# Kernel optimization log

Measured on AMD Instinct MI355X. Metric: run time of the kernel, lower is better.

Reference implementation:

```python
import jax, jax.numpy as jnp
import numpy as np

KERNEL_SIZE = 5
KERNEL_NUM = 64
STRIDE = 1
PRIOR_VAR = 1.0


def setup_inputs() -> dict:
    key = jax.random.key(0)
    k1, k2 = jax.random.split(key)
    mu_in = jax.random.normal(k1, (128, 128, 128, 3), dtype=jnp.float32)
    # init: normal stddev 0.05 for w_mu, constant -4.6 for w_sigma
    w_mu = 0.05 * jax.random.normal(k2, (KERNEL_SIZE, KERNEL_SIZE, 3, KERNEL_NUM), dtype=jnp.float32)
    w_sigma = jnp.full((KERNEL_NUM,), -4.6, dtype=jnp.float32)
    return {"mu_in": mu_in, "w_mu": w_mu, "w_sigma": w_sigma}


def kl_regularizer_conv(mu, logvar):
    k = mu.shape[-1]
    mu2 = mu.reshape(-1, k)              # [k*k*C, kernel_num]
    n = mu2.shape[0]
    kl = -jnp.mean(1.0 + logvar
                   - jnp.log1p(jnp.exp(logvar)) / PRIOR_VAR
                   - jnp.sum(jnp.square(mu2), axis=0) / (n * PRIOR_VAR))
    kl = jnp.where(jnp.isnan(kl), jnp.float32(1e-05), kl)
    kl = jnp.where(jnp.isinf(kl), jnp.float32(1e-05), kl)
    return kl


def reference(mu_in, w_mu, w_sigma):
    B, H, W, C = mu_in.shape
    ks = KERNEL_SIZE
    kl_conv = kl_regularizer_conv(w_mu, w_sigma)
    w_sigma_2 = jnp.log1p(jnp.exp(w_sigma))  # softplus

    dn = ('NHWC', 'HWIO', 'NHWC')
    mu_out = jax.lax.conv_general_dilated(
        mu_in, w_mu, window_strides=(STRIDE, STRIDE), padding='VALID',
        dimension_numbers=dn)  # [B, Ho, Wo, kernel_num]

    # Per-patch sum of squares == sum-pool conv over squared input summed over C
    # (mathematically identical to extract_patches -> square -> sum, no im2col blowup)
    sq = jnp.sum(jnp.square(mu_in), axis=-1, keepdims=True)  # [B,H,W,1]
    ones_k = jnp.ones((ks, ks, 1, 1), dtype=mu_in.dtype)
    patch_ss = jax.lax.conv_general_dilated(
        sq, ones_k, window_strides=(STRIDE, STRIDE), padding='VALID',
        dimension_numbers=dn)  # [B, Ho, Wo, 1]
    x_dim = jnp.float32(ks * ks * C)
    # broadcast: softplus(w_sigma)[kn] * (sum_sq / x_dim)[B,Ho,Wo,1]
    Sigma_out = w_sigma_2 * (patch_ss / x_dim)  # [B, Ho, Wo, kernel_num]

    Ho = mu_out.shape[1]
    Sigma_out = Sigma_out.reshape(B, Ho, Ho, KERNEL_NUM)
    return (mu_out, Sigma_out, kl_conv)
```

## Files before the change

kernel.cpp:

```cpp
#include <hip/hip_runtime.h>
#include <hip/hip_bf16.h>
#include <math.h>

#define KS 5
#define CIN 3
#define KN 64
#define HIN 128
#define HO 124
#define ROWF (HIN * CIN)
#define NOUT (128LL * 124 * 124 * 64)
#define KP 104

typedef short bfrag8 __attribute__((ext_vector_type(8)));
typedef float ffrag4 __attribute__((ext_vector_type(4)));

__device__ __forceinline__ unsigned short f2bf(float f) {
    union { float f; unsigned u; } x;
    x.f = f;
    unsigned r = x.u + 0x7fffu + ((x.u >> 16) & 1u);
    return (unsigned short)(r >> 16);
}

__global__ void prep_kernel(const float* __restrict__ w_mu,
                            const float* __restrict__ w_sigma,
                            unsigned short* __restrict__ w_bf,
                            float* __restrict__ sp_out) {
    const int tid = threadIdx.x;
    const int n = tid >> 2;
    const int kbase = (tid & 3) * 26;
#pragma unroll
    for (int kk = 0; kk < 26; ++kk) {
        const int k = kbase + kk;
        float v = 0.f;
        if (k < 80) {
            const int r = k >> 4, t = k & 15;
            if (t < 15) v = w_mu[(r * 15 + t) * KN + n];
        }
        w_bf[n * KP + k] = f2bf(v);
    }
    if (tid < KN) sp_out[tid] = log1pf(expf(w_sigma[tid]));
}

__global__ void kl_kernel(const float* __restrict__ w_mu,
                          const float* __restrict__ w_sigma,
                          float* __restrict__ out_kl) {
    int kn = threadIdx.x;
    float s = 0.f;
#pragma unroll
    for (int i = 0; i < 75; ++i) {
        float m = w_mu[i * KN + kn];
        s = fmaf(m, m, s);
    }
    float lv = w_sigma[kn];
    float sp = log1pf(expf(lv));
    float val = 1.0f + lv - sp - s * (1.0f / 75.0f);
#pragma unroll
    for (int off = 32; off > 0; off >>= 1) val += __shfl_down(val, off);
    if (kn == 0) {
        float kl = -(val / 64.0f);
        if (isnan(kl) || isinf(kl)) kl = 1e-5f;
        out_kl[0] = kl;
    }
}

__global__ __launch_bounds__(256, 3) void conv_kernel(
    const float* __restrict__ mu_in,
    const unsigned short* __restrict__ w_bf,
    const float* __restrict__ sp_in,
    float* __restrict__ mu_out,
    float* __restrict__ sig_out) {

    __shared__ __align__(16) float s_in[1952];
    __shared__ __align__(16) unsigned short s_x[128 * KP];
    __shared__ __align__(16) unsigned short s_w[KN * KP];
    __shared__ float s_sp[KN];
    __shared__ float s_cs[HIN];
    __shared__ float s_ssn[HIN];

    const int bid = blockIdx.x;
    const int b = bid / HO;
    const int ho = bid % HO;
    const int tid = threadIdx.x;

    const float* src = mu_in + (size_t)(b * HIN + ho) * ROWF;
    for (int i = tid; i < 480; i += 256)
        reinterpret_cast<float4*>(s_in)[i] =
            reinterpret_cast<const float4*>(src)[i];
    if (tid < 32) s_in[1920 + tid] = 0.f;
    for (int i = tid; i < 832; i += 256)
        reinterpret_cast<float4*>(s_w)[i] =
            reinterpret_cast<const float4*>(w_bf)[i];
    if (tid < KN) s_sp[tid] = sp_in[tid];
    __syncthreads();

    if (tid < HIN) {
        float cs = 0.f;
#pragma unroll
        for (int r = 0; r < KS; ++r)
#pragma unroll
            for (int c = 0; c < CIN; ++c) {
                float v = s_in[r * ROWF + tid * CIN + c];
                cs = fmaf(v, v, cs);
            }
        s_cs[tid] = cs;
    }
    __syncthreads();

    if (tid < HIN) {
        float v = 0.f;
        if (tid < HO)
            v = (s_cs[tid] + s_cs[tid + 1] + s_cs[tid + 2] + s_cs[tid + 3] +
                 s_cs[tid + 4]) * (1.0f / 75.0f);
        s_ssn[tid] = v;
    }
    for (int i = tid; i < 640; i += 256) {
        const int r = i >> 7;
        const int wo = i & 127;
        const float* p = &s_in[r * ROWF + wo * CIN];
        unsigned u[8];
#pragma unroll
        for (int j = 0; j < 8; ++j)
            u[j] = (unsigned)f2bf(p[2 * j]) | ((unsigned)f2bf(p[2 * j + 1]) << 16);
        uint4* dst = reinterpret_cast<uint4*>(&s_x[wo * KP + r * 16]);
        dst[0] = make_uint4(u[0], u[1], u[2], u[3]);
        dst[1] = make_uint4(u[4], u[5], u[6], u[7]);
    }
    for (int i = tid; i < 1024; i += 256) {
        const int wo = i >> 3, j = i & 7;
        reinterpret_cast<unsigned*>(s_x)[wo * (KP / 2) + 40 + j] = 0u;
    }
    __syncthreads();

    const int lane = tid & 63;
    const int wid = tid >> 6;
    const int llo = lane & 15;
    const int lhi = lane >> 4;

    bfrag8 afr[4][3];
#pragma unroll
    for (int mt = 0; mt < 4; ++mt)
#pragma unroll
        for (int ks = 0; ks < 3; ++ks)
            afr[mt][ks] = *reinterpret_cast<const bfrag8*>(
                &s_w[(mt * 16 + llo) * KP + ks * 32 + lhi * 8]);

    ffrag4 acc[2][4];
#pragma unroll
    for (int nt = 0; nt < 2; ++nt)
#pragma unroll
        for (int mt = 0; mt < 4; ++mt) acc[nt][mt] = (ffrag4){0.f, 0.f, 0.f, 0.f};

#pragma unroll
    for (int nt = 0; nt < 2; ++nt) {
        const int wo = (wid * 2 + nt) * 16 + llo;
#pragma unroll
        for (int ks = 0; ks < 3; ++ks) {
            bfrag8 bfr = *reinterpret_cast<const bfrag8*>(
                &s_x[wo * KP + ks * 32 + lhi * 8]);
#pragma unroll
            for (int mt = 0; mt < 4; ++mt)
                acc[nt][mt] = __builtin_amdgcn_mfma_f32_16x16x32_bf16(
                    afr[mt][ks], bfr, acc[nt][mt], 0, 0, 0);
        }
    }

    float4 sp4[4];
#pragma unroll
    for (int mt = 0; mt < 4; ++mt)
        sp4[mt] = *reinterpret_cast<const float4*>(&s_sp[mt * 16 + lhi * 4]);

    const size_t orow = (size_t)(b * HO + ho) * (size_t)(HO * KN);
#pragma unroll
    for (int nt = 0; nt < 2; ++nt) {
        const int wo = (wid * 2 + nt) * 16 + llo;
        if (wo < HO) {
            const float ssn = s_ssn[wo];
            const size_t obase = orow + (size_t)wo * KN;
#pragma unroll
            for (int mt = 0; mt < 4; ++mt) {
                const int knb = mt * 16 + lhi * 4;
                *reinterpret_cast<float4*>(&mu_out[obase + knb]) =
                    make_float4(acc[nt][mt][0], acc[nt][mt][1], acc[nt][mt][2],
                                acc[nt][mt][3]);
                *reinterpret_cast<float4*>(&sig_out[obase + knb]) =
                    make_float4(sp4[mt].x * ssn, sp4[mt].y * ssn,
                                sp4[mt].z * ssn, sp4[mt].w * ssn);
            }
        }
    }
}

extern "C" void kernel_launch(void* const* d_in, const int* in_sizes, int n_in,
                              void* d_out, int out_size, void* d_ws,
                              size_t ws_size, hipStream_t stream) {
    const float* mu_in = (const float*)d_in[0];
    const float* w_mu = (const float*)d_in[1];
    const float* w_sigma = (const float*)d_in[2];
    float* out = (float*)d_out;

    float* mu_out = out;
    float* sig_out = out + NOUT;
    float* kl_out = out + 2 * NOUT;

    unsigned short* w_bf = (unsigned short*)d_ws;
    float* sp_ws = (float*)((char*)d_ws + KN * KP * 2);

    prep_kernel<<<1, 256, 0, stream>>>(w_mu, w_sigma, w_bf, sp_ws);
    conv_kernel<<<128 * HO, 256, 0, stream>>>(mu_in, w_bf, sp_ws, mu_out,
                                              sig_out);
    kl_kernel<<<1, 64, 0, stream>>>(w_mu, w_sigma, kl_out);
}
```

Baseline: 248.0 us.

## Compute four output rows per block with shared 8-row bf16 image tile

Each block now handles four output rows and stages eight input rows once as a compact, XOR-swizzled bf16 tile. This replaces the per-output-row im2col buffer, so each input row is converted once and reused across five kernel rows. Weight fragments are loaded straight from global memory instead of through shared memory. Launch bounds rise to 4 blocks per CU and the grid shrinks, which amortises setup but gives fewer, longer blocks whose output is still dominated by store bandwidth.

```diff
diff --git a/kernel.cpp b/kernel.cpp
--- a/kernel.cpp
+++ b/kernel.cpp
@@ -2,14 +2,11 @@
 #include <hip/hip_bf16.h>
 #include <math.h>
 
-#define KS 5
-#define CIN 3
 #define KN 64
-#define HIN 128
 #define HO 124
-#define ROWF (HIN * CIN)
+#define KP 104
 #define NOUT (128LL * 124 * 124 * 64)
-#define KP 104
+#define NG 31
 
 typedef short bfrag8 __attribute__((ext_vector_type(8)));
 typedef float ffrag4 __attribute__((ext_vector_type(4)));
@@ -19,6 +16,13 @@
     x.f = f;
     unsigned r = x.u + 0x7fffu + ((x.u >> 16) & 1u);
     return (unsigned short)(r >> 16);
+}
+__device__ __forceinline__ unsigned pack2(float a, float b) {
+    return (unsigned)f2bf(a) | ((unsigned)f2bf(b) << 16);
+}
+
+__device__ __forceinline__ int im_off(int row, int wo, int half) {
+    return (((row * 128 + wo) * 32) + half * 16) ^ (((wo >> 2) & 7) << 4);
 }
 
 __global__ void prep_kernel(const float* __restrict__ w_mu,
@@ -63,74 +67,69 @@
     }
 }
 
-__global__ __launch_bounds__(256, 3) void conv_kernel(
+template <int OFF>
+__device__ __forceinline__ void im_fill(const float* __restrict__ mu_in,
+                                        unsigned short* s_im, int b, int ho0,
+                                        int lane, int wo) {
+#pragma unroll
+    for (int j = 0; j < 4; ++j) {
+        const int row = ((lane >> 5) << 2) + j;
+        uint4* dst0 =
+            reinterpret_cast<uint4*>((char*)s_im + im_off(row, wo, 0));
+        uint4* dst1 =
+            reinterpret_cast<uint4*>((char*)s_im + im_off(row, wo, 1));
+        if (wo >= 124) {
+            *dst0 = make_uint4(0u, 0u, 0u, 0u);
+            *dst1 = make_uint4(0u, 0u, 0u, 0u);
+            continue;
+        }
+        const float* p =
+            mu_in + ((size_t)(b * 128 + ho0 + row) * 384 + wo * 3 - OFF);
+        float w[20];
+        float4 f;
+        f = reinterpret_cast<const float4*>(p)[0];
+        w[0] = f.x; w[1] = f.y; w[2] = f.z; w[3] = f.w;
+        f = reinterpret_cast<const float4*>(p)[1];
+        w[4] = f.x; w[5] = f.y; w[6] = f.z; w[7] = f.w;
+        f = reinterpret_cast<const float4*>(p)[2];
+        w[8] = f.x; w[9] = f.y; w[10] = f.z; w[11] = f.w;
+        f = reinterpret_cast<const float4*>(p)[3];
+        w[12] = f.x; w[13] = f.y; w[14] = f.z; w[15] = f.w;
+        if (OFF >= 2) {
+            f = reinterpret_cast<const float4*>(p)[4];
+            w[16] = f.x; w[17] = f.y; w[18] = f.z; w[19] = f.w;
+        } else {
+            w[16] = 0.f; w[17] = 0.f; w[18] = 0.f; w[19] = 0.f;
+        }
+        unsigned u0 = pack2(w[OFF + 0], w[OFF + 1]);
+        unsigned u1 = pack2(w[OFF + 2], w[OFF + 3]);
+        unsigned u2 = pack2(w[OFF + 4], w[OFF + 5]);
+        unsigned u3 = pack2(w[OFF + 6], w[OFF + 7]);
+        unsigned u4 = pack2(w[OFF + 8], w[OFF + 9]);
+        unsigned u5 = pack2(w[OFF + 10], w[OFF + 11]);
+        unsigned u6 = pack2(w[OFF + 12], w[OFF + 13]);
+        unsigned u7 = pack2(w[OFF + 14], 0.0f);
+        *dst0 = make_uint4(u0, u1, u2, u3);
+        *dst1 = make_uint4(u4, u5, u6, u7);
+    }
+}
+
+__global__ __launch_bounds__(256, 4) void conv_kernel(
     const float* __restrict__ mu_in,
     const unsigned short* __restrict__ w_bf,
     const float* __restrict__ sp_in,
     float* __restrict__ mu_out,
     float* __restrict__ sig_out) {
 
-    __shared__ __align__(16) float s_in[1952];
-    __shared__ __align__(16) unsigned short s_x[128 * KP];
-    __shared__ __align__(16) unsigned short s_w[KN * KP];
+    __shared__ __align__(16) unsigned short s_im[8 * 128 * 16];
+    __shared__ __align__(16) float s_cs[8 * 128];
+    __shared__ float s_ssn[4 * 128];
     __shared__ float s_sp[KN];
-    __shared__ float s_cs[HIN];
-    __shared__ float s_ssn[HIN];
 
     const int bid = blockIdx.x;
-    const int b = bid / HO;
-    const int ho = bid % HO;
+    const int b = bid / NG;
+    const int ho0 = (bid % NG) * 4;
     const int tid = threadIdx.x;
-
-    const float* src = mu_in + (size_t)(b * HIN + ho) * ROWF;
-    for (int i = tid; i < 480; i += 256)
-        reinterpret_cast<float4*>(s_in)[i] =
-            reinterpret_cast<const float4*>(src)[i];
-    if (tid < 32) s_in[1920 + tid] = 0.f;
-    for (int i = tid; i < 832; i += 256)
-        reinterpret_cast<float4*>(s_w)[i] =
-            reinterpret_cast<const float4*>(w_bf)[i];
-    if (tid < KN) s_sp[tid] = sp_in[tid];
-    __syncthreads();
-
-    if (tid < HIN) {
-        float cs = 0.f;
-#pragma unroll
-        for (int r = 0; r < KS; ++r)
-#pragma unroll
-            for (int c = 0; c < CIN; ++c) {
-                float v = s_in[r * ROWF + tid * CIN + c];
-                cs = fmaf(v, v, cs);
-            }
-        s_cs[tid] = cs;
-    }
-    __syncthreads();
-
-    if (tid < HIN) {
-        float v = 0.f;
-        if (tid < HO)
-            v = (s_cs[tid] + s_cs[tid + 1] + s_cs[tid + 2] + s_cs[tid + 3] +
-                 s_cs[tid + 4]) * (1.0f / 75.0f);
-        s_ssn[tid] = v;
-    }
-    for (int i = tid; i < 640; i += 256) {
-        const int r = i >> 7;
-        const int wo = i & 127;
-        const float* p = &s_in[r * ROWF + wo * CIN];
-        unsigned u[8];
-#pragma unroll
-        for (int j = 0; j < 8; ++j)
-            u[j] = (unsigned)f2bf(p[2 * j]) | ((unsigned)f2bf(p[2 * j + 1]) << 16);
-        uint4* dst = reinterpret_cast<uint4*>(&s_x[wo * KP + r * 16]);
-        dst[0] = make_uint4(u[0], u[1], u[2], u[3]);
-        dst[1] = make_uint4(u[4], u[5], u[6], u[7]);
-    }
-    for (int i = tid; i < 1024; i += 256) {
-        const int wo = i >> 3, j = i & 7;
-        reinterpret_cast<unsigned*>(s_x)[wo * (KP / 2) + 40 + j] = 0u;
-    }
-    __syncthreads();
-
     const int lane = tid & 63;
     const int wid = tid >> 6;
     const int llo = lane & 15;
@@ -142,49 +141,97 @@
 #pragma unroll
         for (int ks = 0; ks < 3; ++ks)
             afr[mt][ks] = *reinterpret_cast<const bfrag8*>(
-                &s_w[(mt * 16 + llo) * KP + ks * 32 + lhi * 8]);
+                &w_bf[(mt * 16 + llo) * KP + ks * 32 + lhi * 8]);
+    if (tid < KN) s_sp[tid] = sp_in[tid];
+
+    {
+        const int r = tid >> 5;
+        const int c4 = (tid & 31) << 2;
+        const float* p = mu_in + ((size_t)(b * 128 + ho0 + r) * 384 + c4 * 3);
+        float4 f0 = reinterpret_cast<const float4*>(p)[0];
+        float4 f1 = reinterpret_cast<const float4*>(p)[1];
+        float4 f2 = reinterpret_cast<const float4*>(p)[2];
+        float4 cs;
+        cs.x = f0.x * f0.x + f0.y * f0.y + f0.z * f0.z;
+        cs.y = f0.w * f0.w + f1.x * f1.x + f1.y * f1.y;
+        cs.z = f1.z * f1.z + f1.w * f1.w + f2.x * f2.x;
+        cs.w = f2.y * f2.y + f2.z * f2.z + f2.w * f2.w;
+        *reinterpret_cast<float4*>(&s_cs[r * 128 + c4]) = cs;
+    }
+
+    {
+        const int wo = wid + ((lane & 31) << 2);
+        switch (wid) {
+            case 0: im_fill<0>(mu_in, s_im, b, ho0, lane, wo); break;
+            case 1: im_fill<3>(mu_in, s_im, b, ho0, lane, wo); break;
+            case 2: im_fill<2>(mu_in, s_im, b, ho0, lane, wo); break;
+            default: im_fill<1>(mu_in, s_im, b, ho0, lane, wo); break;
+        }
+    }
+    __syncthreads();
+
+    for (int i = tid; i < 512; i += 256) {
+        const int hl = i >> 7, wo = i & 127;
+        float v = 0.f;
+        if (wo < HO) {
+            float s = 0.f;
+#pragma unroll
+            for (int r = 0; r < 5; ++r)
+#pragma unroll
+                for (int d = 0; d < 5; ++d) s += s_cs[(hl + r) * 128 + wo + d];
+            v = s * (1.0f / 75.0f);
+        }
+        s_ssn[hl * 128 + wo] = v;
+    }
+    __syncthreads();
 
     ffrag4 acc[2][4];
 #pragma unroll
-    for (int nt = 0; nt < 2; ++nt)
-#pragma unroll
-        for (int mt = 0; mt < 4; ++mt) acc[nt][mt] = (ffrag4){0.f, 0.f, 0.f, 0.f};
-
-#pragma unroll
-    for (int nt = 0; nt < 2; ++nt) {
-        const int wo = (wid * 2 + nt) * 16 + llo;
-#pragma unroll
-        for (int ks = 0; ks < 3; ++ks) {
-            bfrag8 bfr = *reinterpret_cast<const bfrag8*>(
-                &s_x[wo * KP + ks * 32 + lhi * 8]);
+    for (int hl = 0; hl < 4; ++hl) {
+#pragma unroll
+        for (int nt = 0; nt < 2; ++nt)
 #pragma unroll
             for (int mt = 0; mt < 4; ++mt)
-                acc[nt][mt] = __builtin_amdgcn_mfma_f32_16x16x32_bf16(
-                    afr[mt][ks], bfr, acc[nt][mt], 0, 0, 0);
-        }
-    }
-
-    float4 sp4[4];
-#pragma unroll
-    for (int mt = 0; mt < 4; ++mt)
-        sp4[mt] = *reinterpret_cast<const float4*>(&s_sp[mt * 16 + lhi * 4]);
-
-    const size_t orow = (size_t)(b * HO + ho) * (size_t)(HO * KN);
-#pragma unroll
-    for (int nt = 0; nt < 2; ++nt) {
-        const int wo = (wid * 2 + nt) * 16 + llo;
-        if (wo < HO) {
-            const float ssn = s_ssn[wo];
-            const size_t obase = orow + (size_t)wo * KN;
-#pragma unroll
-            for (int mt = 0; mt < 4; ++mt) {
-                const int knb = mt * 16 + lhi * 4;
-                *reinterpret_cast<float4*>(&mu_out[obase + knb]) =
-                    make_float4(acc[nt][mt][0], acc[nt][mt][1], acc[nt][mt][2],
-                                acc[nt][mt][3]);
-                *reinterpret_cast<float4*>(&sig_out[obase + knb]) =
-                    make_float4(sp4[mt].x * ssn, sp4[mt].y * ssn,
-                                sp4[mt].z * ssn, sp4[mt].w * ssn);
+                acc[nt][mt] = (ffrag4){0.f, 0.f, 0.f, 0.f};
+
+#pragma unroll
+        for (int nt = 0; nt < 2; ++nt) {
+            const int wo = (wid * 2 + nt) * 16 + llo;
+#pragma unroll
+            for (int ks = 0; ks < 3; ++ks) {
+                const int k0 = ks * 32 + lhi * 8;
+                const int r = k0 >> 4;
+                bfrag8 bfr = (bfrag8){0, 0, 0, 0, 0, 0, 0, 0};
+                if (r < 5) {
+                    bfr = *reinterpret_cast<const bfrag8*>(
+                        (char*)s_im + im_off(hl + r, wo, (k0 & 15) >> 3));
+                }
+#pragma unroll
+                for (int mt = 0; mt < 4; ++mt)
+                    acc[nt][mt] = __builtin_amdgcn_mfma_f32_16x16x32_bf16(
+                        afr[mt][ks], bfr, acc[nt][mt], 0, 0, 0);
+            }
+        }
+
+        const size_t orow = (size_t)(b * HO + ho0 + hl) * (size_t)(HO * KN);
+#pragma unroll
+        for (int nt = 0; nt < 2; ++nt) {
+            const int wo = (wid * 2 + nt) * 16 + llo;
+            if (wo < HO) {
+                const float ssn = s_ssn[hl * 128 + wo];
+                const size_t obase = orow + (size_t)wo * KN;
+#pragma unroll
+                for (int mt = 0; mt < 4; ++mt) {
+                    const int knb = mt * 16 + lhi * 4;
+                    const float4 sp4 =
+                        *reinterpret_cast<const float4*>(&s_sp[knb]);
+                    *reinterpret_cast<float4*>(&mu_out[obase + knb]) =
+                        make_float4(acc[nt][mt][0], acc[nt][mt][1],
+                                    acc[nt][mt][2], acc[nt][mt][3]);
+                    *reinterpret_cast<float4*>(&sig_out[obase + knb]) =
+                        make_float4(sp4.x * ssn, sp4.y * ssn, sp4.z * ssn,
+                                    sp4.w * ssn);
+                }
             }
         }
     }
@@ -206,7 +253,7 @@
     float* sp_ws = (float*)((char*)d_ws + KN * KP * 2);
 
     prep_kernel<<<1, 256, 0, stream>>>(w_mu, w_sigma, w_bf, sp_ws);
-    conv_kernel<<<128 * HO, 256, 0, stream>>>(mu_in, w_bf, sp_ws, mu_out,
+    conv_kernel<<<128 * NG, 256, 0, stream>>>(mu_in, w_bf, sp_ws, mu_out,
                                               sig_out);
     kl_kernel<<<1, 64, 0, stream>>>(w_mu, w_sigma, kl_out);
 }
```

New measurement: 242.4 us. -2.3%, faster.
